# Kernel optimization log

Hardware: AMD Instinct MI355X
Metric: run time of the kernel (lower is better)

The kernel has to match this reference:

```python
import jax, jax.numpy as jnp
import numpy as np

BS, SL, INDIM, D, H = 2, 2048, 1024, 64, 16
DH = D * H


def _rotation_buffers(sl, units):
    # int rotation_values branch: values=arange(sl), min_lam=1, max_lam=1000
    half = units // 2
    min_lam, max_lam = 1.0, 1000.0
    theta = min_lam / (2.0 * np.pi) * (max_lam / min_lam) ** (2.0 * np.arange(half) / units)
    pos = np.arange(sl, dtype=np.float64)[:, None] / theta[None]  # [sl, half]
    # tile([...,2]).reshape == repeat each entry twice along last dim -> [sl, units]
    rcos = np.repeat(np.cos(pos), 2, axis=-1).astype(np.float32)
    rsin = np.repeat(np.sin(pos), 2, axis=-1).astype(np.float32)
    return jnp.asarray(rcos), jnp.asarray(rsin)


def setup_inputs() -> dict:
    key = jax.random.key(0)
    ks = jax.random.split(key, 8)
    s = 0.02
    x = jax.random.normal(ks[0], (BS, SL, INDIM), jnp.float32)
    mask = jnp.zeros((BS, SL), jnp.float32)  # subtracted from logits; zeros = no masking
    Wqkv = jax.random.normal(ks[1], (INDIM, 3 * DH), jnp.float32) * s
    bqkv = jnp.zeros((3 * DH,), jnp.float32)
    Wo = jax.random.normal(ks[2], (DH, INDIM), jnp.float32) * s
    bo = jnp.zeros((INDIM,), jnp.float32)
    Wg = jax.random.normal(ks[3], (INDIM, DH), jnp.float32) * s
    bg = jnp.zeros((DH,), jnp.float32)
    Wb = jax.random.normal(ks[4], (INDIM, H), jnp.float32) * s
    bb = jnp.zeros((H,), jnp.float32)
    alphaq = jnp.zeros((), jnp.float32)
    alphak = jnp.zeros((), jnp.float32)
    alphav = jnp.zeros((), jnp.float32)
    rcos, rsin = _rotation_buffers(SL, D)
    return dict(x=x, mask=mask, Wqkv=Wqkv, bqkv=bqkv, Wo=Wo, bo=bo, Wg=Wg, bg=bg,
                Wb=Wb, bb=bb, alphaq=alphaq, alphak=alphak, alphav=alphav,
                rcos=rcos, rsin=rsin)


def _rotate(X, cos, sin_even):
    # Faithful to the in-place torch code:
    #   X_ = X*cos; X_[...,::2] += -sin[...,::2]*X_[...,1::2];
    #   X_[...,1::2] += sin[...,::2]*X_[...,::2]   (uses UPDATED even lanes)
    Xc = X * cos
    even = Xc[..., 0::2] - sin_even * Xc[..., 1::2]
    odd = Xc[..., 1::2] + sin_even * even
    return jnp.stack([even, odd], axis=-1).reshape(X.shape)


def reference(x, mask, Wqkv, bqkv, Wo, bo, Wg, bg, Wb, bb, alphaq, alphak, alphav, rcos, rsin):
    bs, sl, _ = x.shape
    qkv = x @ Wqkv + bqkv  # [bs, sl, 3*DH]
    Q, K, V = jnp.split(qkv, 3, axis=-1)
    # split last dim as (d, h) and move heads out: [bs, h, sl, d]
    def split_heads(t):
        return t.reshape(bs, sl, D, H).transpose(0, 3, 1, 2)
    Q = split_heads(Q) * jax.nn.sigmoid(alphaq)
    K = split_heads(K) * jax.nn.sigmoid(alphak)
    V = split_heads(V) * jax.nn.sigmoid(alphav)
    cos = rcos[:sl]            # [sl, d]
    sin_even = rsin[:sl, 0::2]  # [sl, d/2]
    Q = _rotate(Q, cos, sin_even)
    K = _rotate(K, cos, sin_even)
    scale = D ** (-0.5)
    QK = scale * jnp.einsum('bhqd,bhkd->bhqk', Q, K)  # [bs,h,sl,sl]
    # 'regular' bias: Wb(x) -> [bs,sl,h] -> [bs,h,1,sl] broadcast over queries
    B = (x @ Wb + bb)
    QK = QK + jnp.transpose(B, (0, 2, 1))[:, :, None, :]
    QK = QK - mask[:, None, None, :]
    w = jax.nn.softmax(QK, axis=-1)
    att = jnp.einsum('bhqk,bhkd->bhqd', w, V)  # [bs,h,sl,d]
    # sigmoid gate, split the same (d,h) way
    G = jax.nn.sigmoid(x @ Wg + bg).reshape(bs, sl, D, H).transpose(0, 3, 1, 2)
    att = att * G
    # merge heads back as (d, h) -> [bs, sl, d*h]
    att = att.transpose(0, 2, 3, 1).reshape(bs, sl, DH)
    resid = att @ Wo + bo
    return x + resid  # identity shortcut (out_units == indim), dropout=0
```

## Files before the change

### kernel.cpp

```cpp
#include <hip/hip_runtime.h>
#include <cstdint>

typedef unsigned short u16;
typedef unsigned int   u32;
typedef __bf16 bf16x8 __attribute__((ext_vector_type(8)));
typedef u16    u16x8  __attribute__((ext_vector_type(8)));
typedef float  f32x4  __attribute__((ext_vector_type(4)));
typedef float  f32x16 __attribute__((ext_vector_type(16)));
typedef u32    u32x2v __attribute__((ext_vector_type(2)));
typedef __attribute__((address_space(3))) void lds_void;
typedef __attribute__((address_space(1))) void gl_void;

#define GLDS16(gsrc, ldst) \
  __builtin_amdgcn_global_load_lds((gl_void*)(gsrc), (lds_void*)(ldst), 16, 0, 0)

#define DEV __device__ __forceinline__

DEV u16 f2bf(float f) {
  uint32_t u = __float_as_uint(f);
  u += 0x7fff + ((u >> 16) & 1);
  return (u16)(u >> 16);
}
DEV float bf2f(u16 h) { return __uint_as_float(((uint32_t)h) << 16); }
DEV float sigm(float x) { return 1.0f / (1.0f + __expf(-x)); }
DEV u32 shx32(u32 v) { return (u32)__shfl_xor((int)v, 32, 64); }

__global__ __launch_bounds__(256) void cvtx_k(const float* __restrict__ x, u16* __restrict__ xb) {
  int i = blockIdx.x * 256 + threadIdx.x;
  float4 v = ((const float4*)x)[i];
  ushort4 o;
  o.x = f2bf(v.x); o.y = f2bf(v.y); o.z = f2bf(v.z); o.w = f2bf(v.w);
  ((ushort4*)xb)[i] = o;
}

template <int PERM>
__global__ __launch_bounds__(256) void wtransp_k(const float* __restrict__ W, u16* __restrict__ Wt,
                                                 int K, int N) {
  __shared__ float tile[32][33];
  int kt = blockIdx.x, nt = blockIdx.y;
  int t = threadIdx.x;
  int r = t >> 5, c = t & 31;
#pragma unroll
  for (int i = 0; i < 4; ++i)
    tile[r + i * 8][c] = W[(size_t)(kt * 32 + r + i * 8) * N + nt * 32 + c];
  __syncthreads();
#pragma unroll
  for (int i = 0; i < 4; ++i) {
    int ko = kt * 32 + c;
    int kdst = PERM ? ((ko & 15) * 64 + (ko >> 4)) : ko;
    Wt[(size_t)(nt * 32 + r + i * 8) * K + kdst] = f2bf(tile[c][r + i * 8]);
  }
}

__global__ __launch_bounds__(64) void biasb_k(const float* __restrict__ x, const float* __restrict__ Wb,
                                              const float* __restrict__ bb, const float* __restrict__ mask,
                                              float* __restrict__ bmT) {
  int row = blockIdx.x;
  int l = threadIdx.x;
  const float* xr = x + (size_t)row * 1024;
  float acc[16];
#pragma unroll
  for (int h = 0; h < 16; ++h) acc[h] = 0.f;
  for (int it = 0; it < 16; ++it) {
    int k = l + it * 64;
    float xv = xr[k];
    const float4* wr = (const float4*)(Wb + k * 16);
#pragma unroll
    for (int q = 0; q < 4; ++q) {
      float4 wv = wr[q];
      acc[q * 4 + 0] += xv * wv.x; acc[q * 4 + 1] += xv * wv.y;
      acc[q * 4 + 2] += xv * wv.z; acc[q * 4 + 3] += xv * wv.w;
    }
  }
#pragma unroll
  for (int h = 0; h < 16; ++h) {
    float v = acc[h];
#pragma unroll
    for (int m = 32; m >= 1; m >>= 1) v += __shfl_xor(v, m, 64);
    acc[h] = v;
  }
  if (l < 16) {
    int b = row >> 11, s = row & 2047;
    bmT[(size_t)(b * 16 + l) * 2048 + s] = acc[l] + bb[l] - mask[row];
  }
}

template <int EPI, int ALAY>
__global__ __launch_bounds__(256) void gemm_k(const u16* __restrict__ A, const u16* __restrict__ Bt,
                                              const float* __restrict__ bias, const float* __restrict__ addsrc,
                                              void* __restrict__ outp, int M, int N, int K) {
  __shared__ u16 As[128 * 32];
  __shared__ u16 Bs[128 * 32];
  const int t = threadIdx.x, w = t >> 6, l = t & 63;
  const int lr = l & 15, lg = l >> 4;
  const int bm = blockIdx.x, bn = blockIdx.y;
  const int wr = w >> 1, wc = w & 1;
  f32x4 acc[4][4] = {};
  const int nk = K >> 5;
  for (int kt = 0; kt < nk; ++kt) {
    if (kt) __syncthreads();
#pragma unroll
    for (int r = 0; r < 2; ++r) {
      int L = r * 256 + t;
      int arow = bm * 128 + (L >> 2), ak = kt * 32 + (L & 3) * 8;
      size_t aoff;
      if (ALAY == 0) aoff = (size_t)arow * K + ak;
      else aoff = ((size_t)((arow >> 11) * 16 + (ak >> 6)) * 2048 + (arow & 2047)) * 64 + (ak & 63);
      GLDS16(A + aoff, &As[(r * 256 + w * 64) * 8]);
      GLDS16(Bt + (size_t)(bn * 128 + (L >> 2)) * K + (kt * 32 + (L & 3) * 8),
             &Bs[(r * 256 + w * 64) * 8]);
    }
    __syncthreads();
    bf16x8 af[4], bfr[4];
#pragma unroll
    for (int m = 0; m < 4; ++m) af[m] = *(const bf16x8*)&As[(wr * 64 + m * 16 + lr) * 32 + lg * 8];
#pragma unroll
    for (int n = 0; n < 4; ++n) bfr[n] = *(const bf16x8*)&Bs[(wc * 64 + n * 16 + lr) * 32 + lg * 8];
#pragma unroll
    for (int m = 0; m < 4; ++m)
#pragma unroll
      for (int n = 0; n < 4; ++n)
        acc[m][n] = __builtin_amdgcn_mfma_f32_16x16x32_bf16(af[m], bfr[n], acc[m][n], 0, 0, 0);
  }
#pragma unroll
  for (int m = 0; m < 4; ++m)
#pragma unroll
    for (int n = 0; n < 4; ++n) {
      int col = bn * 128 + wc * 64 + n * 16 + lr;
      float bv = bias[col];
#pragma unroll
      for (int rg = 0; rg < 4; ++rg) {
        int row = bm * 128 + wr * 64 + m * 16 + lg * 4 + rg;
        float v = acc[m][n][rg] + bv;
        if (EPI == 0) ((u16*)outp)[(size_t)row * N + col] = f2bf(v);
        else if (EPI == 1) ((float*)outp)[(size_t)row * N + col] = v + addsrc[(size_t)row * N + col];
        else {
          int b2 = row >> 11, s2 = row & 2047;
          ((u16*)outp)[((size_t)(b2 * 16 + (col & 15)) * 2048 + s2) * 64 + (col >> 4)] = f2bf(sigm(v));
        }
      }
    }
}

__global__ __launch_bounds__(256) void relayout_k(const u16* __restrict__ qkv,
    const float* __restrict__ rcos, const float* __restrict__ rsin,
    const float* __restrict__ aq, const float* __restrict__ ak, const float* __restrict__ av,
    u16* __restrict__ Qh, u16* __restrict__ Kh, u16* __restrict__ Vh) {
  int row = blockIdx.x;
  int b = row >> 11, s = row & 2047;
  int t = threadIdx.x;
  float sq = sigm(*aq) * 0.125f, sk = sigm(*ak), sv = sigm(*av);
#pragma unroll
  for (int which = 0; which < 2; ++which) {
    const u16* src = qkv + (size_t)row * 3072 + which * 1024;
    float sc = which ? sk : sq;
    u16* dst = which ? Kh : Qh;
#pragma unroll
    for (int rep = 0; rep < 2; ++rep) {
      int task = t + rep * 256;
      int h = task >> 5, i = task & 31;
      float c = rcos[s * 64 + 2 * i];
      float sn = rsin[s * 64 + 2 * i];
      float xe = bf2f(src[(2 * i) * 16 + h]) * sc;
      float xo = bf2f(src[(2 * i + 1) * 16 + h]) * sc;
      float e = c * xe - sn * (c * xo);
      float o = c * xo + sn * e;
      uint32_t pk = (uint32_t)f2bf(e) | ((uint32_t)f2bf(o) << 16);
      *(uint32_t*)&dst[((size_t)(b * 16 + h) * 2048 + s) * 64 + 2 * i] = pk;
    }
  }
  {
    const u16* src = qkv + (size_t)row * 3072 + 2048;
    int h = t >> 4, d0 = (t & 15) * 4;
    ushort4 o4;
    o4.x = f2bf(bf2f(src[(d0 + 0) * 16 + h]) * sv);
    o4.y = f2bf(bf2f(src[(d0 + 1) * 16 + h]) * sv);
    o4.z = f2bf(bf2f(src[(d0 + 2) * 16 + h]) * sv);
    o4.w = f2bf(bf2f(src[(d0 + 3) * 16 + h]) * sv);
    *(ushort4*)&Vh[((size_t)(b * 16 + h) * 2048 + s) * 64 + d0] = o4;
  }
}

__global__ __launch_bounds__(256) void attn2_k(const u16* __restrict__ Qh, const u16* __restrict__ Kh,
    const u16* __restrict__ Vh, const float* __restrict__ bmT, const u16* __restrict__ gh,
    u16* __restrict__ attg2) {
  __shared__ u16 smem[8192];
  u16* Ks = smem;
  u16* VTs = smem + 4096;
  const int t = threadIdx.x, w = t >> 6, l = t & 63;
  const int q32 = l & 31, hi = l >> 5;
  const int bh = blockIdx.x, qt = blockIdx.y;
  const int q0w = qt * 128 + w * 32;

  bf16x8 qf[4];
  {
    const u16* qbase = Qh + ((size_t)bh * 2048 + q0w + q32) * 64 + hi * 8;
#pragma unroll
    for (int ks = 0; ks < 4; ++ks) qf[ks] = *(const bf16x8*)(qbase + ks * 16);
  }
  f32x16 o0 = {}, o1 = {};
  float mi = -1e30f, li = 0.f;

  for (int kt = 0; kt < 32; ++kt) {
    if (kt) __syncthreads();
#pragma unroll
    for (int r = 0; r < 2; ++r) {
      int L = r * 256 + t;
      int krow = L >> 3, kc = L & 7;
      GLDS16(Kh + ((size_t)bh * 2048 + kt * 64 + krow) * 64 + ((kc ^ (krow & 7)) * 8),
             &Ks[(r * 256 + w * 64) * 8]);
    }
    {
      int kp = t >> 3, dc = t & 7;
      const u16* vsrc = Vh + ((size_t)bh * 2048 + kt * 64 + kp * 2) * 64 + dc * 8;
      u16x8 v0 = *(const u16x8*)vsrc;
      u16x8 v1 = *(const u16x8*)(vsrc + 64);
#pragma unroll
      for (int j = 0; j < 8; ++j) {
        int d = dc * 8 + j;
        int sw = (d & 7) ^ ((d >> 3) & 7);
        *(u32*)((char*)VTs + d * 128 + ((kp * 4) ^ (sw << 4))) = (u32)v0[j] | ((u32)v1[j] << 16);
      }
    }
    __syncthreads();
    float bv0 = bmT[(size_t)bh * 2048 + kt * 64 + q32];
    float bv1 = bmT[(size_t)bh * 2048 + kt * 64 + 32 + q32];
#pragma unroll
    for (int sub = 0; sub < 2; ++sub) {
      f32x16 s = {};
#pragma unroll
      for (int ks = 0; ks < 4; ++ks) {
        bf16x8 kf = *(const bf16x8*)((const char*)Ks + (sub * 32 + q32) * 128 +
                                     (((2 * ks + hi) ^ (q32 & 7)) << 4));
        s = __builtin_amdgcn_mfma_f32_32x32x16_bf16(kf, qf[ks], s, 0, 0, 0);
      }
      {
        union { u32 wd[4]; bf16x8 v; } Ab = {}, Bb = {};
        Ab.wd[0] = hi ? 0u : (u32)f2bf(sub ? bv1 : bv0);
        Bb.wd[0] = hi ? 0u : 0x3F80u;
        s = __builtin_amdgcn_mfma_f32_32x32x16_bf16(Ab.v, Bb.v, s, 0, 0, 0);
      }
      float tm = s[0];
#pragma unroll
      for (int r = 1; r < 16; ++r) tm = fmaxf(tm, s[r]);
      tm = fmaxf(tm, __shfl_xor(tm, 32, 64));
      float mn = fmaxf(mi, tm);
      float fac = __expf(mi - mn);
      mi = mn;
      li *= fac;
#pragma unroll
      for (int r = 0; r < 16; ++r) { o0[r] *= fac; o1[r] *= fac; }
      float p[16];
      float sum = 0.f;
#pragma unroll
      for (int r = 0; r < 16; ++r) { p[r] = __expf(s[r] - mi); sum += p[r]; }
      li += sum;
      u32 c[8], sc[8];
#pragma unroll
      for (int i = 0; i < 8; ++i)
        asm("v_cvt_pk_bf16_f32 %0, %1, %2" : "=v"(c[i]) : "v"(p[2 * i]), "v"(p[2 * i + 1]));
#pragma unroll
      for (int i = 0; i < 8; ++i) sc[i] = shx32(c[i]);
      union { u32 wd[4]; bf16x8 v; } pf[2];
      pf[0].wd[0] = hi ? sc[2] : c[0];
      pf[0].wd[1] = hi ? sc[3] : c[1];
      pf[0].wd[2] = hi ? c[2] : sc[0];
      pf[0].wd[3] = hi ? c[3] : sc[1];
      pf[1].wd[0] = hi ? sc[6] : c[4];
      pf[1].wd[1] = hi ? sc[7] : c[5];
      pf[1].wd[2] = hi ? c[6] : sc[4];
      pf[1].wd[3] = hi ? c[7] : sc[5];
#pragma unroll
      for (int ks2 = 0; ks2 < 2; ++ks2) {
        int chunk = sub * 4 + ks2 * 2 + hi;
        {
          int d = q32;
          int sw = (d & 7) ^ ((d >> 3) & 7);
          bf16x8 vf = *(const bf16x8*)((const char*)VTs + d * 128 + ((chunk ^ sw) << 4));
          o0 = __builtin_amdgcn_mfma_f32_32x32x16_bf16(vf, pf[ks2].v, o0, 0, 0, 0);
        }
        {
          int d = 32 + q32;
          int sw = (d & 7) ^ ((d >> 3) & 7);
          bf16x8 vf = *(const bf16x8*)((const char*)VTs + d * 128 + ((chunk ^ sw) << 4));
          o1 = __builtin_amdgcn_mfma_f32_32x32x16_bf16(vf, pf[ks2].v, o1, 0, 0, 0);
        }
      }
    }
  }
  li += __shfl_xor(li, 32, 64);
  float inv = 1.f / li;
#pragma unroll
  for (int r = 0; r < 16; ++r) { o0[r] *= inv; o1[r] *= inv; }

  __syncthreads();
  {
    char* ob = (char*)smem + w * 4096;
#pragma unroll
    for (int dt = 0; dt < 2; ++dt) {
#pragma unroll
      for (int rq = 0; rq < 4; ++rq) {
        int dbase = rq * 8 + hi * 4 + dt * 32;
        float e0 = dt ? o1[rq * 4 + 0] : o0[rq * 4 + 0];
        float e1 = dt ? o1[rq * 4 + 1] : o0[rq * 4 + 1];
        float e2 = dt ? o1[rq * 4 + 2] : o0[rq * 4 + 2];
        float e3 = dt ? o1[rq * 4 + 3] : o0[rq * 4 + 3];
        u32 lo = (u32)f2bf(e0) | ((u32)f2bf(e1) << 16);
        u32 h2 = (u32)f2bf(e2) | ((u32)f2bf(e3) << 16);
        u32x2v val = {lo, h2};
        *(u32x2v*)(ob + q32 * 128 + ((dbase * 2) ^ ((q32 & 7) << 4))) = val;
      }
    }
  }
  {
    const u16* gbase = gh + ((size_t)bh * 2048 + q0w) * 64;
    u16* abase = attg2 + ((size_t)bh * 2048 + q0w) * 64;
    const char* ob = (const char*)smem + w * 4096;
#pragma unroll
    for (int cc = 0; cc < 4; ++cc) {
      int off16 = cc * 64 + l;
      int q = off16 >> 3;
      int inner = (off16 & 7) << 4;
      u16x8 ov = *(const u16x8*)(ob + q * 128 + (inner ^ ((q & 7) << 4)));
      u16x8 gv = *(const u16x8*)(gbase + off16 * 8);
      u16x8 outv;
#pragma unroll
      for (int j = 0; j < 8; ++j) outv[j] = f2bf(bf2f(ov[j]) * bf2f(gv[j]));
      *(u16x8*)(abase + off16 * 8) = outv;
    }
  }
}

extern "C" void kernel_launch(void* const* d_in, const int* in_sizes, int n_in,
                              void* d_out, int out_size, void* d_ws, size_t ws_size,
                              hipStream_t stream) {
  (void)in_sizes; (void)n_in; (void)out_size; (void)ws_size;
  const float* x    = (const float*)d_in[0];
  const float* mask = (const float*)d_in[1];
  const float* Wqkv = (const float*)d_in[2];
  const float* bqkv = (const float*)d_in[3];
  const float* Wo   = (const float*)d_in[4];
  const float* bo   = (const float*)d_in[5];
  const float* Wg   = (const float*)d_in[6];
  const float* bg   = (const float*)d_in[7];
  const float* Wb   = (const float*)d_in[8];
  const float* bb   = (const float*)d_in[9];
  const float* aq   = (const float*)d_in[10];
  const float* ak   = (const float*)d_in[11];
  const float* av   = (const float*)d_in[12];
  const float* rcos = (const float*)d_in[13];
  const float* rsin = (const float*)d_in[14];
  float* out = (float*)d_out;

  char* ws = (char*)d_ws;
  size_t o = 0;
  u16* x_bf   = (u16*)(ws + o); o += (size_t)4096 * 1024 * 2;
  u16* wqkv_t = (u16*)(ws + o); o += (size_t)3072 * 1024 * 2;
  u16* wg_t   = (u16*)(ws + o); o += (size_t)1024 * 1024 * 2;
  u16* wo_t2  = (u16*)(ws + o); o += (size_t)1024 * 1024 * 2;
  u16* qkv_b  = (u16*)(ws + o); o += (size_t)4096 * 3072 * 2;
  u16* gh     = (u16*)(ws + o); o += (size_t)4096 * 1024 * 2;
  u16* Qh     = (u16*)(ws + o); o += (size_t)32 * 2048 * 64 * 2;
  u16* Kh     = (u16*)(ws + o); o += (size_t)32 * 2048 * 64 * 2;
  u16* Vh     = (u16*)(ws + o); o += (size_t)32 * 2048 * 64 * 2;
  float* bmT  = (float*)(ws + o); o += (size_t)32 * 2048 * 4;
  u16* attg2  = (u16*)(ws + o); o += (size_t)4096 * 1024 * 2;

  cvtx_k<<<4096, 256, 0, stream>>>(x, x_bf);
  wtransp_k<0><<<dim3(32, 96), 256, 0, stream>>>(Wqkv, wqkv_t, 1024, 3072);
  wtransp_k<0><<<dim3(32, 32), 256, 0, stream>>>(Wg, wg_t, 1024, 1024);
  wtransp_k<1><<<dim3(32, 32), 256, 0, stream>>>(Wo, wo_t2, 1024, 1024);
  biasb_k<<<4096, 64, 0, stream>>>(x, Wb, bb, mask, bmT);
  gemm_k<0, 0><<<dim3(32, 24), 256, 0, stream>>>(x_bf, wqkv_t, bqkv, nullptr, qkv_b, 4096, 3072, 1024);
  gemm_k<2, 0><<<dim3(32, 8), 256, 0, stream>>>(x_bf, wg_t, bg, nullptr, gh, 4096, 1024, 1024);
  relayout_k<<<4096, 256, 0, stream>>>(qkv_b, rcos, rsin, aq, ak, av, Qh, Kh, Vh);
  attn2_k<<<dim3(32, 16), 256, 0, stream>>>(Qh, Kh, Vh, bmT, gh, attg2);
  gemm_k<1, 1><<<dim3(32, 8), 256, 0, stream>>>(attg2, wo_t2, bo, x, out, 4096, 1024, 1024);
}
```

Measured before the change: 345.3 us.

## Fuse QKV and gate GEMMs, split KV across warps in attention, retile output GEMM

Concatenates the QKV and gate weights so one GEMM produces both, and moves the gate head-relayout into the relayout kernel. Attention is rewritten so each block handles 64 queries with two warp groups covering separate KV halves; their softmax states are merged through LDS, and blocks are remapped for XCD locality. Softmax now uses exp2 with log2e folded into the Q scale and bias, skips rescaling when the max grows by 8 or less, and uses permlane32_swap in place of shuffles. The output GEMM uses 64-row tiles to launch more blocks. The lazy rescale bounds the exp2 argument, which adds some numerical risk, and the split-KV merge adds extra LDS traffic and a barrier.

```diff
diff --git a/kernel.cpp b/kernel.cpp
--- a/kernel.cpp
+++ b/kernel.cpp
@@ -15,6 +15,7 @@
   __builtin_amdgcn_global_load_lds((gl_void*)(gsrc), (lds_void*)(ldst), 16, 0, 0)
 
 #define DEV __device__ __forceinline__
+#define LOG2E 1.4426950408889634f
 
 DEV u16 f2bf(float f) {
   uint32_t u = __float_as_uint(f);
@@ -23,7 +24,6 @@
 }
 DEV float bf2f(u16 h) { return __uint_as_float(((uint32_t)h) << 16); }
 DEV float sigm(float x) { return 1.0f / (1.0f + __expf(-x)); }
-DEV u32 shx32(u32 v) { return (u32)__shfl_xor((int)v, 32, 64); }
 
 __global__ __launch_bounds__(256) void cvtx_k(const float* __restrict__ x, u16* __restrict__ xb) {
   int i = blockIdx.x * 256 + threadIdx.x;
@@ -81,14 +81,13 @@
   }
   if (l < 16) {
     int b = row >> 11, s = row & 2047;
-    bmT[(size_t)(b * 16 + l) * 2048 + s] = acc[l] + bb[l] - mask[row];
-  }
-}
-
-template <int EPI, int ALAY>
-__global__ __launch_bounds__(256) void gemm_k(const u16* __restrict__ A, const u16* __restrict__ Bt,
-                                              const float* __restrict__ bias, const float* __restrict__ addsrc,
-                                              void* __restrict__ outp, int M, int N, int K) {
+    bmT[(size_t)(b * 16 + l) * 2048 + s] = (acc[l] + bb[l] - mask[row]) * LOG2E;
+  }
+}
+
+__global__ __launch_bounds__(256) void gemmF_k(const u16* __restrict__ A, const u16* __restrict__ Bt,
+                                               const float* __restrict__ bqkv, const float* __restrict__ bg,
+                                               u16* __restrict__ qkvb, u16* __restrict__ gh_rm) {
   __shared__ u16 As[128 * 32];
   __shared__ u16 Bs[128 * 32];
   const int t = threadIdx.x, w = t >> 6, l = t & 63;
@@ -96,18 +95,14 @@
   const int bm = blockIdx.x, bn = blockIdx.y;
   const int wr = w >> 1, wc = w & 1;
   f32x4 acc[4][4] = {};
-  const int nk = K >> 5;
-  for (int kt = 0; kt < nk; ++kt) {
+  for (int kt = 0; kt < 32; ++kt) {
     if (kt) __syncthreads();
 #pragma unroll
     for (int r = 0; r < 2; ++r) {
       int L = r * 256 + t;
-      int arow = bm * 128 + (L >> 2), ak = kt * 32 + (L & 3) * 8;
-      size_t aoff;
-      if (ALAY == 0) aoff = (size_t)arow * K + ak;
-      else aoff = ((size_t)((arow >> 11) * 16 + (ak >> 6)) * 2048 + (arow & 2047)) * 64 + (ak & 63);
-      GLDS16(A + aoff, &As[(r * 256 + w * 64) * 8]);
-      GLDS16(Bt + (size_t)(bn * 128 + (L >> 2)) * K + (kt * 32 + (L & 3) * 8),
+      GLDS16(A + (size_t)(bm * 128 + (L >> 2)) * 1024 + (kt * 32 + (L & 3) * 8),
+             &As[(r * 256 + w * 64) * 8]);
+      GLDS16(Bt + (size_t)(bn * 128 + (L >> 2)) * 1024 + (kt * 32 + (L & 3) * 8),
              &Bs[(r * 256 + w * 64) * 8]);
     }
     __syncthreads();
@@ -127,50 +122,49 @@
 #pragma unroll
     for (int n = 0; n < 4; ++n) {
       int col = bn * 128 + wc * 64 + n * 16 + lr;
-      float bv = bias[col];
+      float bv = (bn < 24) ? bqkv[col] : bg[col - 3072];
 #pragma unroll
       for (int rg = 0; rg < 4; ++rg) {
         int row = bm * 128 + wr * 64 + m * 16 + lg * 4 + rg;
         float v = acc[m][n][rg] + bv;
-        if (EPI == 0) ((u16*)outp)[(size_t)row * N + col] = f2bf(v);
-        else if (EPI == 1) ((float*)outp)[(size_t)row * N + col] = v + addsrc[(size_t)row * N + col];
-        else {
-          int b2 = row >> 11, s2 = row & 2047;
-          ((u16*)outp)[((size_t)(b2 * 16 + (col & 15)) * 2048 + s2) * 64 + (col >> 4)] = f2bf(sigm(v));
-        }
+        if (bn < 24) qkvb[(size_t)row * 3072 + col] = f2bf(v);
+        else         gh_rm[(size_t)row * 1024 + (col - 3072)] = f2bf(sigm(v));
       }
     }
 }
 
 __global__ __launch_bounds__(256) void relayout_k(const u16* __restrict__ qkv,
+    const u16* __restrict__ gh_rm,
     const float* __restrict__ rcos, const float* __restrict__ rsin,
     const float* __restrict__ aq, const float* __restrict__ ak, const float* __restrict__ av,
-    u16* __restrict__ Qh, u16* __restrict__ Kh, u16* __restrict__ Vh) {
+    u16* __restrict__ Qh, u16* __restrict__ Kh, u16* __restrict__ Vh, u16* __restrict__ Gh) {
   int row = blockIdx.x;
   int b = row >> 11, s = row & 2047;
   int t = threadIdx.x;
-  float sq = sigm(*aq) * 0.125f, sk = sigm(*ak), sv = sigm(*av);
-#pragma unroll
-  for (int which = 0; which < 2; ++which) {
-    const u16* src = qkv + (size_t)row * 3072 + which * 1024;
+  float sq = sigm(*aq) * 0.125f * LOG2E, sk = sigm(*ak), sv = sigm(*av);
+  const u16* qrow = qkv + (size_t)row * 3072;
+  if (t < 128) {
+    int which = t >> 6;
+    int idx = t & 63;
+    int hoct = idx & 1, dp = idx >> 1;
+    const u16* src = qrow + which * 1024;
     float sc = which ? sk : sq;
     u16* dst = which ? Kh : Qh;
-#pragma unroll
-    for (int rep = 0; rep < 2; ++rep) {
-      int task = t + rep * 256;
-      int h = task >> 5, i = task & 31;
-      float c = rcos[s * 64 + 2 * i];
-      float sn = rsin[s * 64 + 2 * i];
-      float xe = bf2f(src[(2 * i) * 16 + h]) * sc;
-      float xo = bf2f(src[(2 * i + 1) * 16 + h]) * sc;
-      float e = c * xe - sn * (c * xo);
-      float o = c * xo + sn * e;
-      uint32_t pk = (uint32_t)f2bf(e) | ((uint32_t)f2bf(o) << 16);
-      *(uint32_t*)&dst[((size_t)(b * 16 + h) * 2048 + s) * 64 + 2 * i] = pk;
+    float cc = rcos[s * 64 + 2 * dp];
+    float sn = rsin[s * 64 + 2 * dp];
+    u16x8 Av = *(const u16x8*)(src + dp * 32 + hoct * 8);
+    u16x8 Bv = *(const u16x8*)(src + dp * 32 + 16 + hoct * 8);
+#pragma unroll
+    for (int j = 0; j < 8; ++j) {
+      float xe = bf2f(Av[j]) * sc, xo = bf2f(Bv[j]) * sc;
+      float e = cc * xe - sn * (cc * xo);
+      float o2 = cc * xo + sn * e;
+      u32 pk = (u32)f2bf(e) | ((u32)f2bf(o2) << 16);
+      *(u32*)&dst[((size_t)(b * 16 + hoct * 8 + j) * 2048 + s) * 64 + 2 * dp] = pk;
     }
   }
   {
-    const u16* src = qkv + (size_t)row * 3072 + 2048;
+    const u16* src = qrow + 2048;
     int h = t >> 4, d0 = (t & 15) * 4;
     ushort4 o4;
     o4.x = f2bf(bf2f(src[(d0 + 0) * 16 + h]) * sv);
@@ -179,18 +173,34 @@
     o4.w = f2bf(bf2f(src[(d0 + 3) * 16 + h]) * sv);
     *(ushort4*)&Vh[((size_t)(b * 16 + h) * 2048 + s) * 64 + d0] = o4;
   }
-}
-
-__global__ __launch_bounds__(256) void attn2_k(const u16* __restrict__ Qh, const u16* __restrict__ Kh,
-    const u16* __restrict__ Vh, const float* __restrict__ bmT, const u16* __restrict__ gh,
+  {
+    const u16* src = gh_rm + (size_t)row * 1024;
+    int h = t >> 4, d0 = (t & 15) * 4;
+    ushort4 o4;
+    o4.x = src[(d0 + 0) * 16 + h];
+    o4.y = src[(d0 + 1) * 16 + h];
+    o4.z = src[(d0 + 2) * 16 + h];
+    o4.w = src[(d0 + 3) * 16 + h];
+    *(ushort4*)&Gh[((size_t)(b * 16 + h) * 2048 + s) * 64 + d0] = o4;
+  }
+}
+
+__global__ __launch_bounds__(256, 4) void attn3_k(const u16* __restrict__ Qh, const u16* __restrict__ Kh,
+    const u16* __restrict__ Vh, const float* __restrict__ bmT, const u16* __restrict__ Gh,
     u16* __restrict__ attg2) {
-  __shared__ u16 smem[8192];
-  u16* Ks = smem;
-  u16* VTs = smem + 4096;
+  __shared__ u16 smem[16384];
+  u16* KsA  = smem;
+  u16* VTsA = smem + 4096;
+  u16* KsB  = smem + 8192;
+  u16* VTsB = smem + 12288;
   const int t = threadIdx.x, w = t >> 6, l = t & 63;
   const int q32 = l & 31, hi = l >> 5;
-  const int bh = blockIdx.x, qt = blockIdx.y;
-  const int q0w = qt * 128 + w * 32;
+  const int bid = blockIdx.x;
+  const int xcd = bid & 7, j = bid >> 3;
+  const int bh = xcd * 4 + (j & 3);
+  const int qt64 = j >> 2;
+  const int q32t = w >> 1, kvh = w & 1;
+  const int q0w = qt64 * 64 + q32t * 32;
 
   bf16x8 qf[4];
   {
@@ -201,28 +211,38 @@
   f32x16 o0 = {}, o1 = {};
   float mi = -1e30f, li = 0.f;
 
-  for (int kt = 0; kt < 32; ++kt) {
-    if (kt) __syncthreads();
-#pragma unroll
-    for (int r = 0; r < 2; ++r) {
-      int L = r * 256 + t;
-      int krow = L >> 3, kc = L & 7;
-      GLDS16(Kh + ((size_t)bh * 2048 + kt * 64 + krow) * 64 + ((kc ^ (krow & 7)) * 8),
-             &Ks[(r * 256 + w * 64) * 8]);
-    }
-    {
-      int kp = t >> 3, dc = t & 7;
-      const u16* vsrc = Vh + ((size_t)bh * 2048 + kt * 64 + kp * 2) * 64 + dc * 8;
-      u16x8 v0 = *(const u16x8*)vsrc;
-      u16x8 v1 = *(const u16x8*)(vsrc + 64);
-#pragma unroll
-      for (int j = 0; j < 8; ++j) {
-        int d = dc * 8 + j;
-        int sw = (d & 7) ^ ((d >> 3) & 7);
-        *(u32*)((char*)VTs + d * 128 + ((kp * 4) ^ (sw << 4))) = (u32)v0[j] | ((u32)v1[j] << 16);
+  u16* Ks  = kvh ? KsB : KsA;
+  u16* VTs = kvh ? VTsB : VTsA;
+
+  for (int i = 0; i < 16; ++i) {
+    if (i) __syncthreads();
+#pragma unroll
+    for (int tile = 0; tile < 2; ++tile) {
+      int ktg = tile * 16 + i;
+      u16* KsT  = tile ? KsB : KsA;
+      u16* VTsT = tile ? VTsB : VTsA;
+#pragma unroll
+      for (int r = 0; r < 2; ++r) {
+        int L = r * 256 + t;
+        int krow = L >> 3, kc = L & 7;
+        GLDS16(Kh + ((size_t)bh * 2048 + ktg * 64 + krow) * 64 + ((kc ^ (krow & 7)) * 8),
+               &KsT[(r * 256 + w * 64) * 8]);
+      }
+      {
+        int kp = t >> 3, dc = t & 7;
+        const u16* vsrc = Vh + ((size_t)bh * 2048 + ktg * 64 + kp * 2) * 64 + dc * 8;
+        u16x8 v0 = *(const u16x8*)vsrc;
+        u16x8 v1 = *(const u16x8*)(vsrc + 64);
+#pragma unroll
+        for (int jj = 0; jj < 8; ++jj) {
+          int d = dc * 8 + jj;
+          int sw = (d & 7) ^ ((d >> 3) & 7);
+          *(u32*)((char*)VTsT + d * 128 + ((kp * 4) ^ (sw << 4))) = (u32)v0[jj] | ((u32)v1[jj] << 16);
+        }
       }
     }
     __syncthreads();
+    int kt = kvh * 16 + i;
     float bv0 = bmT[(size_t)bh * 2048 + kt * 64 + q32];
     float bv1 = bmT[(size_t)bh * 2048 + kt * 64 + 32 + q32];
 #pragma unroll
@@ -235,87 +255,108 @@
         s = __builtin_amdgcn_mfma_f32_32x32x16_bf16(kf, qf[ks], s, 0, 0, 0);
       }
       {
+        float bvs = sub ? bv1 : bv0;
+        u32 bvb;
+        asm("v_cvt_pk_bf16_f32 %0, %1, %2" : "=v"(bvb) : "v"(bvs), "v"(0.f));
         union { u32 wd[4]; bf16x8 v; } Ab = {}, Bb = {};
-        Ab.wd[0] = hi ? 0u : (u32)f2bf(sub ? bv1 : bv0);
+        Ab.wd[0] = hi ? 0u : bvb;
         Bb.wd[0] = hi ? 0u : 0x3F80u;
         s = __builtin_amdgcn_mfma_f32_32x32x16_bf16(Ab.v, Bb.v, s, 0, 0, 0);
       }
-      float tm = s[0];
-#pragma unroll
-      for (int r = 1; r < 16; ++r) tm = fmaxf(tm, s[r]);
+      float ma = fmaxf(fmaxf(s[0], s[1]), fmaxf(s[2], s[3]));
+      float mb = fmaxf(fmaxf(s[4], s[5]), fmaxf(s[6], s[7]));
+      float mc = fmaxf(fmaxf(s[8], s[9]), fmaxf(s[10], s[11]));
+      float md = fmaxf(fmaxf(s[12], s[13]), fmaxf(s[14], s[15]));
+      float tm = fmaxf(fmaxf(ma, mb), fmaxf(mc, md));
       tm = fmaxf(tm, __shfl_xor(tm, 32, 64));
-      float mn = fmaxf(mi, tm);
-      float fac = __expf(mi - mn);
-      mi = mn;
-      li *= fac;
-#pragma unroll
-      for (int r = 0; r < 16; ++r) { o0[r] *= fac; o1[r] *= fac; }
+      if (!__all(tm <= mi + 8.f)) {
+        float mn = fmaxf(mi, tm);
+        float fac = exp2f(mi - mn);
+        mi = mn; li *= fac;
+#pragma unroll
+        for (int r = 0; r < 16; ++r) { o0[r] *= fac; o1[r] *= fac; }
+      }
       float p[16];
-      float sum = 0.f;
-#pragma unroll
-      for (int r = 0; r < 16; ++r) { p[r] = __expf(s[r] - mi); sum += p[r]; }
-      li += sum;
-      u32 c[8], sc[8];
-#pragma unroll
-      for (int i = 0; i < 8; ++i)
-        asm("v_cvt_pk_bf16_f32 %0, %1, %2" : "=v"(c[i]) : "v"(p[2 * i]), "v"(p[2 * i + 1]));
-#pragma unroll
-      for (int i = 0; i < 8; ++i) sc[i] = shx32(c[i]);
-      union { u32 wd[4]; bf16x8 v; } pf[2];
-      pf[0].wd[0] = hi ? sc[2] : c[0];
-      pf[0].wd[1] = hi ? sc[3] : c[1];
-      pf[0].wd[2] = hi ? c[2] : sc[0];
-      pf[0].wd[3] = hi ? c[3] : sc[1];
-      pf[1].wd[0] = hi ? sc[6] : c[4];
-      pf[1].wd[1] = hi ? sc[7] : c[5];
-      pf[1].wd[2] = hi ? c[6] : sc[4];
-      pf[1].wd[3] = hi ? c[7] : sc[5];
+#pragma unroll
+      for (int r = 0; r < 16; ++r) p[r] = exp2f(s[r] - mi);
+      float s0 = (p[0] + p[1]) + (p[2] + p[3]);
+      float s1 = (p[4] + p[5]) + (p[6] + p[7]);
+      float s2 = (p[8] + p[9]) + (p[10] + p[11]);
+      float s3 = (p[12] + p[13]) + (p[14] + p[15]);
+      li += (s0 + s1) + (s2 + s3);
+      u32 c[8];
+#pragma unroll
+      for (int i2 = 0; i2 < 8; ++i2)
+        asm("v_cvt_pk_bf16_f32 %0, %1, %2" : "=v"(c[i2]) : "v"(p[2 * i2]), "v"(p[2 * i2 + 1]));
+      asm volatile("v_permlane32_swap_b32 %0, %1" : "+v"(c[0]), "+v"(c[2]));
+      asm volatile("v_permlane32_swap_b32 %0, %1" : "+v"(c[1]), "+v"(c[3]));
+      asm volatile("v_permlane32_swap_b32 %0, %1" : "+v"(c[4]), "+v"(c[6]));
+      asm volatile("v_permlane32_swap_b32 %0, %1" : "+v"(c[5]), "+v"(c[7]));
+      union { u32 wd[4]; bf16x8 v; } pf0, pf1;
+      pf0.wd[0] = c[0]; pf0.wd[1] = c[1]; pf0.wd[2] = c[2]; pf0.wd[3] = c[3];
+      pf1.wd[0] = c[4]; pf1.wd[1] = c[5]; pf1.wd[2] = c[6]; pf1.wd[3] = c[7];
 #pragma unroll
       for (int ks2 = 0; ks2 < 2; ++ks2) {
         int chunk = sub * 4 + ks2 * 2 + hi;
+        const bf16x8* pv = ks2 ? &pf1.v : &pf0.v;
         {
           int d = q32;
           int sw = (d & 7) ^ ((d >> 3) & 7);
           bf16x8 vf = *(const bf16x8*)((const char*)VTs + d * 128 + ((chunk ^ sw) << 4));
-          o0 = __builtin_amdgcn_mfma_f32_32x32x16_bf16(vf, pf[ks2].v, o0, 0, 0, 0);
+          o0 = __builtin_amdgcn_mfma_f32_32x32x16_bf16(vf, *pv, o0, 0, 0, 0);
         }
         {
           int d = 32 + q32;
           int sw = (d & 7) ^ ((d >> 3) & 7);
           bf16x8 vf = *(const bf16x8*)((const char*)VTs + d * 128 + ((chunk ^ sw) << 4));
-          o1 = __builtin_amdgcn_mfma_f32_32x32x16_bf16(vf, pf[ks2].v, o1, 0, 0, 0);
+          o1 = __builtin_amdgcn_mfma_f32_32x32x16_bf16(vf, *pv, o1, 0, 0, 0);
         }
       }
     }
   }
   li += __shfl_xor(li, 32, 64);
-  float inv = 1.f / li;
-#pragma unroll
-  for (int r = 0; r < 16; ++r) { o0[r] *= inv; o1[r] *= inv; }
-
   __syncthreads();
-  {
-    char* ob = (char*)smem + w * 4096;
+  float* Of = (float*)smem + q32t * 2048;
+  float* ml = (float*)smem + 4096;
+  if (kvh == 0) {
+#pragma unroll
+    for (int r = 0; r < 16; ++r) {
+      int d = (r & 3) + 8 * (r >> 2) + 4 * hi;
+      Of[d * 32 + q32] = o0[r];
+      Of[(d + 32) * 32 + q32] = o1[r];
+    }
+    if (hi == 0) { ml[q32t * 64 + q32] = mi; ml[q32t * 64 + 32 + q32] = li; }
+  }
+  __syncthreads();
+  if (kvh == 1) {
+    float m0 = ml[q32t * 64 + q32], l0 = ml[q32t * 64 + 32 + q32];
+    float M = fmaxf(m0, mi);
+    float e0 = exp2f(m0 - M), e1 = exp2f(mi - M);
+    float inv = 1.f / (l0 * e0 + li * e1);
+#pragma unroll
+    for (int r = 0; r < 16; ++r) {
+      int d = (r & 3) + 8 * (r >> 2) + 4 * hi;
+      o0[r] = (Of[d * 32 + q32] * e0 + o0[r] * e1) * inv;
+      o1[r] = (Of[(d + 32) * 32 + q32] * e0 + o1[r] * e1) * inv;
+    }
+    char* ob = (char*)Of;
 #pragma unroll
     for (int dt = 0; dt < 2; ++dt) {
 #pragma unroll
       for (int rq = 0; rq < 4; ++rq) {
         int dbase = rq * 8 + hi * 4 + dt * 32;
-        float e0 = dt ? o1[rq * 4 + 0] : o0[rq * 4 + 0];
-        float e1 = dt ? o1[rq * 4 + 1] : o0[rq * 4 + 1];
-        float e2 = dt ? o1[rq * 4 + 2] : o0[rq * 4 + 2];
-        float e3 = dt ? o1[rq * 4 + 3] : o0[rq * 4 + 3];
-        u32 lo = (u32)f2bf(e0) | ((u32)f2bf(e1) << 16);
-        u32 h2 = (u32)f2bf(e2) | ((u32)f2bf(e3) << 16);
+        float e0v = dt ? o1[rq * 4 + 0] : o0[rq * 4 + 0];
+        float e1v = dt ? o1[rq * 4 + 1] : o0[rq * 4 + 1];
+        float e2v = dt ? o1[rq * 4 + 2] : o0[rq * 4 + 2];
+        float e3v = dt ? o1[rq * 4 + 3] : o0[rq * 4 + 3];
+        u32 lo = (u32)f2bf(e0v) | ((u32)f2bf(e1v) << 16);
+        u32 h2 = (u32)f2bf(e2v) | ((u32)f2bf(e3v) << 16);
         u32x2v val = {lo, h2};
         *(u32x2v*)(ob + q32 * 128 + ((dbase * 2) ^ ((q32 & 7) << 4))) = val;
       }
     }
-  }
-  {
-    const u16* gbase = gh + ((size_t)bh * 2048 + q0w) * 64;
+    const u16* gbase = Gh + ((size_t)bh * 2048 + q0w) * 64;
     u16* abase = attg2 + ((size_t)bh * 2048 + q0w) * 64;
-    const char* ob = (const char*)smem + w * 4096;
 #pragma unroll
     for (int cc = 0; cc < 4; ++cc) {
       int off16 = cc * 64 + l;
@@ -325,10 +366,59 @@
       u16x8 gv = *(const u16x8*)(gbase + off16 * 8);
       u16x8 outv;
 #pragma unroll
-      for (int j = 0; j < 8; ++j) outv[j] = f2bf(bf2f(ov[j]) * bf2f(gv[j]));
+      for (int jj = 0; jj < 8; ++jj) outv[jj] = f2bf(bf2f(ov[jj]) * bf2f(gv[jj]));
       *(u16x8*)(abase + off16 * 8) = outv;
     }
   }
+}
+
+__global__ __launch_bounds__(256) void gemm2_k(const u16* __restrict__ A, const u16* __restrict__ Bt,
+                                               const float* __restrict__ bo, const float* __restrict__ x,
+                                               float* __restrict__ out) {
+  __shared__ u16 As[64 * 32];
+  __shared__ u16 Bs[128 * 32];
+  const int t = threadIdx.x, w = t >> 6, l = t & 63;
+  const int lr = l & 15, lg = l >> 4;
+  const int bm = blockIdx.x, bn = blockIdx.y;
+  const int wr = w >> 1, wc = w & 1;
+  f32x4 acc[2][4] = {};
+  for (int kt = 0; kt < 32; ++kt) {
+    if (kt) __syncthreads();
+    {
+      int arow = bm * 64 + (t >> 2), ak = kt * 32 + (t & 3) * 8;
+      size_t aoff = ((size_t)((arow >> 11) * 16 + (ak >> 6)) * 2048 + (arow & 2047)) * 64 + (ak & 63);
+      GLDS16(A + aoff, &As[w * 64 * 8]);
+    }
+#pragma unroll
+    for (int r = 0; r < 2; ++r) {
+      int L = r * 256 + t;
+      GLDS16(Bt + (size_t)(bn * 128 + (L >> 2)) * 1024 + (kt * 32 + (L & 3) * 8),
+             &Bs[(r * 256 + w * 64) * 8]);
+    }
+    __syncthreads();
+    bf16x8 af[2], bfr[4];
+#pragma unroll
+    for (int m = 0; m < 2; ++m) af[m] = *(const bf16x8*)&As[(wr * 32 + m * 16 + lr) * 32 + lg * 8];
+#pragma unroll
+    for (int n = 0; n < 4; ++n) bfr[n] = *(const bf16x8*)&Bs[(wc * 64 + n * 16 + lr) * 32 + lg * 8];
+#pragma unroll
+    for (int m = 0; m < 2; ++m)
+#pragma unroll
+      for (int n = 0; n < 4; ++n)
+        acc[m][n] = __builtin_amdgcn_mfma_f32_16x16x32_bf16(af[m], bfr[n], acc[m][n], 0, 0, 0);
+  }
+#pragma unroll
+  for (int m = 0; m < 2; ++m)
+#pragma unroll
+    for (int n = 0; n < 4; ++n) {
+      int col = bn * 128 + wc * 64 + n * 16 + lr;
+      float bv = bo[col];
+#pragma unroll
+      for (int rg = 0; rg < 4; ++rg) {
+        int row = bm * 64 + wr * 32 + m * 16 + lg * 4 + rg;
+        out[(size_t)row * 1024 + col] = acc[m][n][rg] + bv + x[(size_t)row * 1024 + col];
+      }
+    }
 }
 
 extern "C" void kernel_launch(void* const* d_in, const int* in_sizes, int n_in,
@@ -355,11 +445,11 @@
   char* ws = (char*)d_ws;
   size_t o = 0;
   u16* x_bf   = (u16*)(ws + o); o += (size_t)4096 * 1024 * 2;
-  u16* wqkv_t = (u16*)(ws + o); o += (size_t)3072 * 1024 * 2;
-  u16* wg_t   = (u16*)(ws + o); o += (size_t)1024 * 1024 * 2;
+  u16* wcat   = (u16*)(ws + o); o += (size_t)4096 * 1024 * 2;
   u16* wo_t2  = (u16*)(ws + o); o += (size_t)1024 * 1024 * 2;
   u16* qkv_b  = (u16*)(ws + o); o += (size_t)4096 * 3072 * 2;
-  u16* gh     = (u16*)(ws + o); o += (size_t)4096 * 1024 * 2;
+  u16* gh_rm  = (u16*)(ws + o); o += (size_t)4096 * 1024 * 2;
+  u16* Gh     = (u16*)(ws + o); o += (size_t)32 * 2048 * 64 * 2;
   u16* Qh     = (u16*)(ws + o); o += (size_t)32 * 2048 * 64 * 2;
   u16* Kh     = (u16*)(ws + o); o += (size_t)32 * 2048 * 64 * 2;
   u16* Vh     = (u16*)(ws + o); o += (size_t)32 * 2048 * 64 * 2;
@@ -367,13 +457,12 @@
   u16* attg2  = (u16*)(ws + o); o += (size_t)4096 * 1024 * 2;
 
   cvtx_k<<<4096, 256, 0, stream>>>(x, x_bf);
-  wtransp_k<0><<<dim3(32, 96), 256, 0, stream>>>(Wqkv, wqkv_t, 1024, 3072);
-  wtransp_k<0><<<dim3(32, 32), 256, 0, stream>>>(Wg, wg_t, 1024, 1024);
+  wtransp_k<0><<<dim3(32, 96), 256, 0, stream>>>(Wqkv, wcat, 1024, 3072);
+  wtransp_k<0><<<dim3(32, 32), 256, 0, stream>>>(Wg, wcat + (size_t)3072 * 1024, 1024, 1024);
   wtransp_k<1><<<dim3(32, 32), 256, 0, stream>>>(Wo, wo_t2, 1024, 1024);
   biasb_k<<<4096, 64, 0, stream>>>(x, Wb, bb, mask, bmT);
-  gemm_k<0, 0><<<dim3(32, 24), 256, 0, stream>>>(x_bf, wqkv_t, bqkv, nullptr, qkv_b, 4096, 3072, 1024);
-  gemm_k<2, 0><<<dim3(32, 8), 256, 0, stream>>>(x_bf, wg_t, bg, nullptr, gh, 4096, 1024, 1024);
-  relayout_k<<<4096, 256, 0, stream>>>(qkv_b, rcos, rsin, aq, ak, av, Qh, Kh, Vh);
-  attn2_k<<<dim3(32, 16), 256, 0, stream>>>(Qh, Kh, Vh, bmT, gh, attg2);
-  gemm_k<1, 1><<<dim3(32, 8), 256, 0, stream>>>(attg2, wo_t2, bo, x, out, 4096, 1024, 1024);
-}
+  gemmF_k<<<dim3(32, 32), 256, 0, stream>>>(x_bf, wcat, bqkv, bg, qkv_b, gh_rm);
+  relayout_k<<<4096, 256, 0, stream>>>(qkv_b, gh_rm, rcos, rsin, aq, ak, av, Qh, Kh, Vh, Gh);
+  attn3_k<<<1024, 256, 0, stream>>>(Qh, Kh, Vh, bmT, Gh, attg2);
+  gemm2_k<<<dim3(64, 8), 256, 0, stream>>>(attg2, wo_t2, bo, x, out);
+}
```

After: 304.3 us. 1.13x faster.
